# Kernel tuning notes

Hardware: AMD Instinct MI355X
Metric: run time of the kernel (lower is better)

## Reference

```python
import jax, jax.numpy as jnp
import numpy as np

N, IN_DIM, H1, NHEAD = 8192, 768, 128, 2
H1T = NHEAD * H1          # 256: each AttentionLayer output dim
H2, H3, OUT = 128, 128, 64
K = H1T + 1 - H2          # 129: conv kernel width
E_PAIRS = 100000
ALPHA = 0.2
NEG = -9e15


def _l2norm(x):
    # F.normalize(p=2, dim=1)
    return x / jnp.maximum(jnp.linalg.norm(x, axis=1, keepdims=True), 1e-12)


def _gat_block(h, adj_mask, a, act):
    # h: [N, D]; a: [2D, 1]; dense NxN GAT attention, masked softmax, aggregate
    D = h.shape[1]
    wh1 = h @ a[:D]            # [N,1]
    wh2 = h @ a[D:]            # [N,1]
    e = act(wh1 + wh2.T)       # [N,N]
    att = jnp.where(adj_mask, e, NEG)
    att = jax.nn.softmax(att, axis=1)   # dropout omitted (eval/deterministic)
    return att @ h             # [N,D]


def _attention_layer(x, adj_mask, W, a, b):
    h = x @ W                  # [N, H1T]
    hp = _gat_block(h, adj_mask, a, lambda z: jax.nn.leaky_relu(z, negative_slope=ALPHA))
    return _l2norm(jax.nn.elu(hp)) + b


def setup_inputs() -> dict:
    key = jax.random.key(0)
    ks = jax.random.split(key, 16)
    g = 1.414

    def xavier(k, shape):
        fan_in, fan_out = shape[-2], shape[-1]
        bound = g * np.sqrt(6.0 / (fan_in + fan_out))
        return jax.random.uniform(k, shape, jnp.float32, -bound, bound)

    x = jax.random.normal(ks[0], (N, IN_DIM), jnp.float32)
    adj = jax.random.randint(ks[1], (N, N), 0, 2, jnp.int32)
    train_sample = jax.random.randint(ks[2], (E_PAIRS, 2), 0, N, jnp.int32)

    return {
        "x": x, "adj": adj, "train_sample": train_sample,
        # per-head GAT params (stacked over heads)
        "head_W": xavier(ks[3], (NHEAD, IN_DIM, H1T)),
        "head_a": xavier(ks[4], (NHEAD, 2 * H1T, 1)),
        "head_b": jnp.zeros((NHEAD, H1T), jnp.float32),
        # Conv attention layer
        "conv_w": jax.random.normal(ks[5], (1, 1, 1, K), jnp.float32) * (1.0 / np.sqrt(K)),
        "conv_cb": jnp.zeros((1,), jnp.float32),
        "conv_a": xavier(ks[6], (2 * H2, 1)),
        "conv_b": jnp.zeros((H2,), jnp.float32),
        # decoder MLPs (stored as [in, out])
        "tf_w1": xavier(ks[7], (H2, H3)), "tf_b1": jnp.zeros((H3,), jnp.float32),
        "tf_w2": xavier(ks[8], (H3, OUT)), "tf_b2": jnp.zeros((OUT,), jnp.float32),
        "tg_w1": xavier(ks[9], (H2, H3)), "tg_b1": jnp.zeros((H3,), jnp.float32),
        "tg_w2": xavier(ks[10], (H3, OUT)), "tg_b2": jnp.zeros((OUT,), jnp.float32),
    }


def reference(x, adj, train_sample, head_W, head_a, head_b,
              conv_w, conv_cb, conv_a, conv_b,
              tf_w1, tf_b1, tf_w2, tf_b2, tg_w1, tg_b1, tg_w2, tg_b2):
    adj_mask = adj > 0

    # Layer 1: mean over attention heads, then elu
    heads = jax.vmap(_attention_layer, in_axes=(None, None, 0, 0, 0))(
        x, adj_mask, head_W, head_a, head_b)           # [NHEAD, N, H1T]
    z = jax.nn.elu(jnp.mean(heads, axis=0))            # [N, H1T]

    # Conv layer: 1x129 conv sliding over feature axis -> [N, H2]
    zi = z[None, None, :, :]                           # [1,1,N,H1T]
    hc = jax.lax.conv_general_dilated(
        zi, conv_w, window_strides=(1, 1), padding="VALID",
        dimension_numbers=("NCHW", "OIHW", "NCHW"))
    h = hc[0, 0] + conv_cb[0]                          # [N, H2]

    hp = _gat_block(h, adj_mask, conv_a, jax.nn.elu)
    embed = _l2norm(jax.nn.elu(hp)) + conv_b           # [N, H2]

    # decoders (dropout p=0.01 omitted for deterministic reference)
    tf = jax.nn.elu(jax.nn.elu(embed @ tf_w1 + tf_b1) @ tf_w2 + tf_b2)
    tg = jax.nn.elu(jax.nn.elu(embed @ tg_w1 + tg_b1) @ tg_w2 + tg_b2)

    pred = jnp.sum(tf[train_sample[:, 0]] * tg[train_sample[:, 1]], axis=1, keepdims=True)
    return pred
```

## Files before the change

kernel.cpp:

```cpp
#include <hip/hip_runtime.h>


typedef _Float16 f16;
typedef _Float16 f16x8 __attribute__((ext_vector_type(8)));
typedef float f32x4 __attribute__((ext_vector_type(4)));

#define DEV __device__ __forceinline__
#define L2E 1.4426950408889634f
#define NN 8192
#define IND 768
#define D1 256
#define DT 512
#define D2 128
#define KC 129
#define EPAIRS 100000

#if __has_builtin(__builtin_amdgcn_exp2f)
#define EXP2(x) __builtin_amdgcn_exp2f(x)
#else
#define EXP2(x) exp2f(x)
#endif

DEV float eluf(float x){ return x > 0.f ? x : EXP2(x*L2E) - 1.f; }

__global__ __launch_bounds__(256) void k_pack(const int4* __restrict__ adj4, unsigned* __restrict__ maskw){
  int idx = blockIdx.x*256 + threadIdx.x;
  int4 v = adj4[idx];
  unsigned n = (unsigned)(v.x > 0) | ((unsigned)(v.y > 0) << 1)
             | ((unsigned)(v.z > 0) << 2) | ((unsigned)(v.w > 0) << 3);
  n |= __shfl_xor(n, 1) << 4;
  n |= __shfl_xor(n, 2) << 8;
  n |= __shfl_xor(n, 4) << 16;
  if ((threadIdx.x & 7) == 0) maskw[idx >> 3] = n;
}

__global__ __launch_bounds__(256) void k_cast_x(const float* __restrict__ x, f16* __restrict__ x16){
  int i = (blockIdx.x*256 + threadIdx.x)*4;
  float4 v = *(const float4*)(x + i);
  union { f16 h[4]; uint2 u; } p;
  p.h[0]=(f16)v.x; p.h[1]=(f16)v.y; p.h[2]=(f16)v.z; p.h[3]=(f16)v.w;
  *(uint2*)(x16 + i) = p.u;
}

__global__ __launch_bounds__(256) void k_wt(const float* __restrict__ W, f16* __restrict__ Wt){
  int np = blockIdx.x; int h = np >> 8, d = np & 255;
  for (int k = threadIdx.x; k < IND; k += 256)
    Wt[(size_t)np*IND + k] = (f16)W[((size_t)h*IND + k)*D1 + d];
}

__global__ __launch_bounds__(256) void k_gemm_h(
    const f16* __restrict__ x16, const f16* __restrict__ Wt,
    const float* __restrict__ head_a,
    f16* __restrict__ hT, float* __restrict__ wh1, float* __restrict__ wh2){
  __shared__ f16 As[64*72];
  __shared__ f16 Bs[128*72];
  int m0 = blockIdx.x*64, n0 = blockIdx.y*128;
  int t = threadIdx.x, lane = t & 63, w = t >> 6;
  int wi = w >> 1, wd = w & 1;
  int rm = lane & 15, qm = (lane >> 4)*8;
  f32x4 acc[2][4] = {};
  for (int k0 = 0; k0 < IND; k0 += 64){
#pragma unroll
    for (int p = 0; p < 2; p++){
      int idx = p*256 + t, r = idx >> 3, cc = (idx & 7)*8;
      *(uint4*)&As[r*72 + cc] = *(const uint4*)&x16[(size_t)(m0 + r)*IND + k0 + cc];
    }
#pragma unroll
    for (int p = 0; p < 4; p++){
      int idx = p*256 + t, r = idx >> 3, cc = (idx & 7)*8;
      *(uint4*)&Bs[r*72 + cc] = *(const uint4*)&Wt[(size_t)(n0 + r)*IND + k0 + cc];
    }
    __syncthreads();
#pragma unroll
    for (int ks = 0; ks < 2; ks++){
      f16x8 a0 = *(const f16x8*)&As[(wi*32 + rm)*72 + ks*32 + qm];
      f16x8 a1 = *(const f16x8*)&As[(wi*32 + 16 + rm)*72 + ks*32 + qm];
#pragma unroll
      for (int fn = 0; fn < 4; fn++){
        f16x8 b = *(const f16x8*)&Bs[(wd*64 + fn*16 + rm)*72 + ks*32 + qm];
        acc[0][fn] = __builtin_amdgcn_mfma_f32_16x16x32_f16(a0, b, acc[0][fn], 0, 0, 0);
        acc[1][fn] = __builtin_amdgcn_mfma_f32_16x16x32_f16(a1, b, acc[1][fn], 0, 0, 0);
      }
    }
    __syncthreads();
  }
  int quad = lane >> 4, cl = lane & 15;
  int head = n0 >> 8;
  float a1v[4], a2v[4];
#pragma unroll
  for (int fn = 0; fn < 4; fn++){
    int d = (n0 & 255) + wd*64 + fn*16 + cl;
    a1v[fn] = head_a[head*DT + d];
    a2v[fn] = head_a[head*DT + D1 + d];
  }
  float p1[2][4], p2[2][4];
#pragma unroll
  for (int fi = 0; fi < 2; fi++){
#pragma unroll
    for (int fn = 0; fn < 4; fn++){
      int npg = n0 + wd*64 + fn*16 + cl;
      int mg = m0 + wi*32 + fi*16 + quad*4;
      union { f16 h[4]; uint2 u; } pk;
#pragma unroll
      for (int reg = 0; reg < 4; reg++) pk.h[reg] = (f16)acc[fi][fn][reg];
      *(uint2*)&hT[(size_t)npg*NN + mg] = pk.u;
    }
#pragma unroll
    for (int reg = 0; reg < 4; reg++){
      float s1 = 0.f, s2 = 0.f;
#pragma unroll
      for (int fn = 0; fn < 4; fn++){ s1 += acc[fi][fn][reg]*a1v[fn]; s2 += acc[fi][fn][reg]*a2v[fn]; }
      p1[fi][reg] = s1; p2[fi][reg] = s2;
    }
  }
#pragma unroll
  for (int o = 1; o < 16; o <<= 1){
#pragma unroll
    for (int fi = 0; fi < 2; fi++)
#pragma unroll
      for (int reg = 0; reg < 4; reg++){
        p1[fi][reg] += __shfl_xor(p1[fi][reg], o);
        p2[fi][reg] += __shfl_xor(p2[fi][reg], o);
      }
  }
  if (cl == 0){
#pragma unroll
    for (int fi = 0; fi < 2; fi++)
#pragma unroll
      for (int reg = 0; reg < 4; reg++){
        int mg = m0 + wi*32 + fi*16 + quad*4 + reg;
        atomicAdd(&wh1[head*NN + mg], p1[fi][reg]);
        atomicAdd(&wh2[head*NN + mg], p2[fi][reg]);
      }
  }
}

__global__ __launch_bounds__(256) void k_gmax(const float* __restrict__ wh2, unsigned* __restrict__ gmax){
  int h = blockIdx.y;
  int i = blockIdx.x*256 + threadIdx.x;
  float v = wh2[h*NN + i];
#pragma unroll
  for (int o = 32; o > 0; o >>= 1) v = fmaxf(v, __shfl_xor(v, o));
  if ((threadIdx.x & 63) == 0){
    unsigned b = __float_as_uint(v);
    unsigned enc = (b & 0x80000000u) ? ~b : (b | 0x80000000u);
    atomicMax(gmax + h, enc);
  }
}

__global__ __launch_bounds__(256) void k_colterms(const float* __restrict__ wh2,
                                                  float* __restrict__ c1, float* __restrict__ c2){
  int i = blockIdx.x*256 + threadIdx.x;
  float v = wh2[i]*L2E;
  c1[i] = v; c2[i] = 0.2f*v;
}

__global__ __launch_bounds__(256) void k_agg_head(
    const f16* __restrict__ hT, const unsigned* __restrict__ maskw,
    const float* __restrict__ wh1, const float* __restrict__ c1,
    const float* __restrict__ c2, const unsigned* __restrict__ gmaxp,
    float* __restrict__ num, float* __restrict__ den){
  __shared__ f16 Hs[256*72];
  __shared__ f16 Ws[64*72];
  __shared__ float rowa[64], rowb[64];
  int head = blockIdx.z;
  int i0 = blockIdx.x*64;
  int jbase = blockIdx.y*4096;
  const f16* hTh = hT + (size_t)head*D1*NN;
  int t = threadIdx.x, lane = t & 63, w = t >> 6;
  int rm = lane & 15, qm = (lane >> 4)*8;
  if (t < 64){
    unsigned e = gmaxp[head];
    float gmax = __uint_as_float((e & 0x80000000u) ? (e ^ 0x80000000u) : ~e);
    float u = wh1[head*NN + i0 + t];
    float sm = u + gmax;
    float M = (sm > 0.f ? sm : 0.2f*sm)*L2E;
    rowa[t] = u*L2E - M;
    rowb[t] = 0.2f*u*L2E - M;
  }
  __syncthreads();
  int si = t >> 2, sjq = (t & 3)*16;
  float ra = rowa[si], rb = rowb[si];
  const float* c1h = c1 + head*NN;
  const float* c2h = c2 + head*NN;
  const unsigned* mrowp = maskw + (size_t)(i0 + si)*(NN/32);
  float rden = 0.f;
  f32x4 acc[4][4] = {};
  for (int j0 = 0; j0 < 4096; j0 += 64){
    int jg = jbase + j0;
#pragma unroll
    for (int p = 0; p < 8; p++){
      int idx = p*256 + t, dr = idx >> 3, cc = (idx & 7)*8;
      *(uint4*)&Hs[dr*72 + cc] = *(const uint4*)&hTh[(size_t)dr*NN + jg + cc];
    }
    unsigned mb = mrowp[(jg + sjq) >> 5] >> (sjq & 31);
    float ca[16], cb[16];
#pragma unroll
    for (int k = 0; k < 4; k++){
      float4 va = *(const float4*)&c1h[jg + sjq + 4*k];
      float4 vb = *(const float4*)&c2h[jg + sjq + 4*k];
      ca[4*k]=va.x; ca[4*k+1]=va.y; ca[4*k+2]=va.z; ca[4*k+3]=va.w;
      cb[4*k]=vb.x; cb[4*k+1]=vb.y; cb[4*k+2]=vb.z; cb[4*k+3]=vb.w;
    }
    f16x8 wlo, whi;
    float dsum = 0.f;
#pragma unroll
    for (int q = 0; q < 16; q++){
      float s1 = ra + ca[q], s2 = rb + cb[q];
      float wv = EXP2(fmaxf(s1, s2));
      wv = ((mb >> q) & 1u) ? wv : 0.f;
      dsum += wv;
      if (q < 8) wlo[q] = (f16)wv; else whi[q - 8] = (f16)wv;
    }
    *(f16x8*)&Ws[si*72 + sjq]     = wlo;
    *(f16x8*)&Ws[si*72 + sjq + 8] = whi;
    dsum += __shfl_xor(dsum, 1);
    dsum += __shfl_xor(dsum, 2);
    rden += dsum;
    __syncthreads();
#pragma unroll
    for (int ks = 0; ks < 2; ks++){
      f16x8 a[4], b[4];
#pragma unroll
      for (int mi = 0; mi < 4; mi++) a[mi] = *(const f16x8*)&Ws[(mi*16 + rm)*72 + ks*32 + qm];
#pragma unroll
      for (int fn = 0; fn < 4; fn++) b[fn] = *(const f16x8*)&Hs[(w*64 + fn*16 + rm)*72 + ks*32 + qm];
#pragma unroll
      for (int mi = 0; mi < 4; mi++)
#pragma unroll
        for (int fn = 0; fn < 4; fn++)
          acc[mi][fn] = __builtin_amdgcn_mfma_f32_16x16x32_f16(a[mi], b[fn], acc[mi][fn], 0, 0, 0);
    }
    __syncthreads();
  }
  if ((t & 3) == 0) atomicAdd(&den[head*NN + i0 + si], rden);
  int quad = lane >> 4, cl = lane & 15;
#pragma unroll
  for (int mi = 0; mi < 4; mi++)
#pragma unroll
    for (int fn = 0; fn < 4; fn++){
      int rr = i0 + mi*16 + quad*4;
      int dc = w*64 + fn*16 + cl;
#pragma unroll
      for (int reg = 0; reg < 4; reg++)
        atomicAdd(&num[((size_t)head*NN + rr + reg)*D1 + dc], acc[mi][fn][reg]);
    }
}

__global__ __launch_bounds__(256) void k_merge_conv(
    const float* __restrict__ num, const float* __restrict__ den,
    const float* __restrict__ head_b, const float* __restrict__ conv_w,
    const float* __restrict__ conv_cb, const float* __restrict__ conv_a,
    f16* __restrict__ gT, float* __restrict__ wc1L, float* __restrict__ wc2L){
  __shared__ float zrow[2][256];
  __shared__ float cw[KC];
  __shared__ float ca[256];
  __shared__ float red[2][2];
  __shared__ float red2[2][2][2];
  int t = threadIdx.x, g = t >> 7, c = t & 127;
  int r = blockIdx.x*2 + g;
  if (t < KC) cw[t] = conv_w[t];
  ca[t] = conv_a[t];
  float zv0 = 0.f, zv1 = 0.f;
#pragma unroll
  for (int h = 0; h < 2; h++){
    const float* nr = num + ((size_t)h*NN + r)*D1;
    float inv = 1.f / den[h*NN + r];
    float e0 = eluf(nr[c]*inv);
    float e1 = eluf(nr[c + 128]*inv);
    float ss = e0*e0 + e1*e1;
#pragma unroll
    for (int o = 32; o > 0; o >>= 1) ss += __shfl_xor(ss, o);
    if ((t & 63) == 0) red[g][(t >> 6) & 1] = ss;
    __syncthreads();
    float invn = 1.f / fmaxf(sqrtf(red[g][0] + red[g][1]), 1e-12f);
    zv0 += e0*invn + head_b[h*D1 + c];
    zv1 += e1*invn + head_b[h*D1 + 128 + c];
    __syncthreads();
  }
  zrow[g][c]       = eluf(0.5f*zv0);
  zrow[g][c + 128] = eluf(0.5f*zv1);
  __syncthreads();
  float s = conv_cb[0];
  for (int k = 0; k < KC; k++) s += zrow[g][c + k]*cw[k];
  gT[(size_t)c*NN + r] = (f16)s;
  float p1 = s*ca[c], p2 = s*ca[128 + c];
#pragma unroll
  for (int o = 32; o > 0; o >>= 1){ p1 += __shfl_xor(p1, o); p2 += __shfl_xor(p2, o); }
  if ((t & 63) == 0){ red2[g][(t >> 6) & 1][0] = p1; red2[g][(t >> 6) & 1][1] = p2; }
  __syncthreads();
  if ((t & 127) == 0){
    wc1L[r] = (red2[g][0][0] + red2[g][1][0])*L2E;
    wc2L[r] = (red2[g][0][1] + red2[g][1][1])*L2E;
  }
}

__global__ __launch_bounds__(256) void k_agg_conv(
    const f16* __restrict__ gT, const unsigned* __restrict__ maskw,
    const float* __restrict__ wc1L, const float* __restrict__ wc2L,
    float* __restrict__ num, float* __restrict__ den){
  __shared__ f16 Hs[128*72];
  __shared__ f16 Ws[64*72];
  __shared__ float rowc[64];
  int i0 = blockIdx.x*64;
  int jbase = blockIdx.y*1024;
  int t = threadIdx.x, lane = t & 63, w = t >> 6;
  int rm = lane & 15, qm = (lane >> 4)*8;
  if (t < 64) rowc[t] = wc1L[i0 + t];
  __syncthreads();
  int si = t >> 2, sjq = (t & 3)*16;
  float ra = rowc[si];
  const unsigned* mrowp = maskw + (size_t)(i0 + si)*(NN/32);
  float rden = 0.f;
  f32x4 acc[4][2] = {};
  for (int j0 = 0; j0 < 1024; j0 += 64){
    int jg = jbase + j0;
#pragma unroll
    for (int p = 0; p < 4; p++){
      int idx = p*256 + t, dr = idx >> 3, cc = (idx & 7)*8;
      *(uint4*)&Hs[dr*72 + cc] = *(const uint4*)&gT[(size_t)dr*NN + jg + cc];
    }
    unsigned mb = mrowp[(jg + sjq) >> 5] >> (sjq & 31);
    float ca[16];
#pragma unroll
    for (int k = 0; k < 4; k++){
      float4 va = *(const float4*)&wc2L[jg + sjq + 4*k];
      ca[4*k]=va.x; ca[4*k+1]=va.y; ca[4*k+2]=va.z; ca[4*k+3]=va.w;
    }
    f16x8 wlo, whi;
    float dsum = 0.f;
#pragma unroll
    for (int q = 0; q < 16; q++){
      float sL = ra + ca[q];
      float t2 = EXP2(sL);
      float wv = sL > 0.f ? t2 : EXP2((t2 - 1.f)*L2E);
      wv = ((mb >> q) & 1u) ? wv : 0.f;
      dsum += wv;
      if (q < 8) wlo[q] = (f16)wv; else whi[q - 8] = (f16)wv;
    }
    *(f16x8*)&Ws[si*72 + sjq]     = wlo;
    *(f16x8*)&Ws[si*72 + sjq + 8] = whi;
    dsum += __shfl_xor(dsum, 1);
    dsum += __shfl_xor(dsum, 2);
    rden += dsum;
    __syncthreads();
#pragma unroll
    for (int ks = 0; ks < 2; ks++){
      f16x8 a[4], b[2];
#pragma unroll
      for (int mi = 0; mi < 4; mi++) a[mi] = *(const f16x8*)&Ws[(mi*16 + rm)*72 + ks*32 + qm];
#pragma unroll
      for (int fn = 0; fn < 2; fn++) b[fn] = *(const f16x8*)&Hs[(w*32 + fn*16 + rm)*72 + ks*32 + qm];
#pragma unroll
      for (int mi = 0; mi < 4; mi++)
#pragma unroll
        for (int fn = 0; fn < 2; fn++)
          acc[mi][fn] = __builtin_amdgcn_mfma_f32_16x16x32_f16(a[mi], b[fn], acc[mi][fn], 0, 0, 0);
    }
    __syncthreads();
  }
  if ((t & 3) == 0) atomicAdd(&den[i0 + si], rden);
  int quad = lane >> 4, cl = lane & 15;
#pragma unroll
  for (int mi = 0; mi < 4; mi++)
#pragma unroll
    for (int fn = 0; fn < 2; fn++){
      int rr = i0 + mi*16 + quad*4;
      int dc = w*32 + fn*16 + cl;
#pragma unroll
      for (int reg = 0; reg < 4; reg++)
        atomicAdd(&num[(size_t)(rr + reg)*D2 + dc], acc[mi][fn][reg]);
    }
}

__global__ __launch_bounds__(256) void k_embed(
    const float* __restrict__ numc, const float* __restrict__ denc,
    const float* __restrict__ conv_b, float* __restrict__ embed){
  __shared__ float red[2][2];
  int t = threadIdx.x, g = t >> 7, c = t & 127;
  int r = blockIdx.x*2 + g;
  float e = eluf(numc[(size_t)r*D2 + c] / denc[r]);
  float ss = e*e;
#pragma unroll
  for (int o = 32; o > 0; o >>= 1) ss += __shfl_xor(ss, o);
  if ((t & 63) == 0) red[g][(t >> 6) & 1] = ss;
  __syncthreads();
  float invn = 1.f / fmaxf(sqrtf(red[g][0] + red[g][1]), 1e-12f);
  embed[(size_t)r*D2 + c] = e*invn + conv_b[c];
}

__global__ __launch_bounds__(256) void k_mlp(
    const float* __restrict__ embed,
    const float* __restrict__ fw1, const float* __restrict__ fb1,
    const float* __restrict__ fw2, const float* __restrict__ fb2,
    const float* __restrict__ gw1, const float* __restrict__ gb1,
    const float* __restrict__ gw2, const float* __restrict__ gb2,
    float* __restrict__ tf, float* __restrict__ tg){
  const float* w1 = blockIdx.y ? gw1 : fw1;
  const float* b1 = blockIdx.y ? gb1 : fb1;
  const float* w2 = blockIdx.y ? gw2 : fw2;
  const float* b2 = blockIdx.y ? gb2 : fb2;
  float* out = blockIdx.y ? tg : tf;
  int t = threadIdx.x;
  int c = t & 127, kh = t >> 7;
  int o = t & 63, kh2 = t >> 6;
  float rw1[64];
#pragma unroll
  for (int i = 0; i < 64; i++) rw1[i] = w1[(kh*64 + i)*128 + c];
  float rw2[32];
#pragma unroll
  for (int i = 0; i < 32; i++) rw2[i] = w2[(kh2*32 + i)*64 + o];
  float bb1 = b1[c], bb2 = b2[o];
  __shared__ float erow[4][128];
  __shared__ float hidp[2][4][128];
  __shared__ float hid[4][128];
  __shared__ float outp[4][4][64];
  int r0 = blockIdx.x*32;
  for (int it = 0; it < 8; it++){
    int rbase = r0 + it*4;
    ((float2*)erow)[t] = ((const float2*)(embed + (size_t)rbase*128))[t];
    __syncthreads();
#pragma unroll
    for (int g = 0; g < 4; g++){
      float s = 0.f;
#pragma unroll
      for (int i = 0; i < 64; i++) s += erow[g][kh*64 + i]*rw1[i];
      hidp[kh][g][c] = s;
    }
    __syncthreads();
#pragma unroll
    for (int gg = 0; gg < 2; gg++){
      int g = kh + 2*gg;
      hid[g][c] = eluf(bb1 + hidp[0][g][c] + hidp[1][g][c]);
    }
    __syncthreads();
#pragma unroll
    for (int g = 0; g < 4; g++){
      float s = 0.f;
#pragma unroll
      for (int i = 0; i < 32; i++) s += hid[g][kh2*32 + i]*rw2[i];
      outp[kh2][g][o] = s;
    }
    __syncthreads();
    { int g = t >> 6;
      out[(size_t)(rbase + g)*64 + o] =
        eluf(bb2 + outp[0][g][o] + outp[1][g][o] + outp[2][g][o] + outp[3][g][o]); }
    __syncthreads();
  }
}

__global__ __launch_bounds__(256) void k_pred(
    const int* __restrict__ ts, const float4* __restrict__ tf4,
    const float4* __restrict__ tg4, float* __restrict__ out){
  int p = blockIdx.x*16 + (threadIdx.x >> 4);
  int l = threadIdx.x & 15;
  int i = ts[2*p], j = ts[2*p + 1];
  float4 a = tf4[(size_t)i*16 + l], b = tg4[(size_t)j*16 + l];
  float v = a.x*b.x + a.y*b.y + a.z*b.z + a.w*b.w;
  v += __shfl_xor(v, 1); v += __shfl_xor(v, 2);
  v += __shfl_xor(v, 4); v += __shfl_xor(v, 8);
  if (l == 0) out[p] = v;
}

#define OFF_MASK  ((size_t)0)
#define OFF_X16   ((size_t)8388608)
#define OFF_WT16  ((size_t)20971520)
#define OFF_HT16  ((size_t)21757952)
#define OFF_WH1   ((size_t)30146560)
#define OFF_WH2   ((size_t)30212096)
#define OFF_C1    ((size_t)30277632)
#define OFF_C2    ((size_t)30343168)
#define OFF_GMAX  ((size_t)30408704)
#define OFF_NUM1  ((size_t)30408960)
#define OFF_DEN1  ((size_t)47186176)
#define OFF_GT16  ((size_t)47251712)
#define OFF_WC1L  ((size_t)49348864)
#define OFF_WC2L  ((size_t)49381632)
#define OFF_NUMC  ((size_t)49414400)
#define OFF_DENC  ((size_t)53608704)
#define OFF_EMB   ((size_t)53641472)
#define OFF_TF    ((size_t)57835776)
#define OFF_TG    ((size_t)59932928)

extern "C" void kernel_launch(void* const* d_in, const int* in_sizes, int n_in,
                              void* d_out, int out_size, void* d_ws, size_t ws_size,
                              hipStream_t stream){
  const float* x      = (const float*)d_in[0];
  const int*   adj    = (const int*)d_in[1];
  const int*   ts     = (const int*)d_in[2];
  const float* head_W = (const float*)d_in[3];
  const float* head_a = (const float*)d_in[4];
  const float* head_b = (const float*)d_in[5];
  const float* conv_w = (const float*)d_in[6];
  const float* conv_cb= (const float*)d_in[7];
  const float* conv_a = (const float*)d_in[8];
  const float* conv_b = (const float*)d_in[9];
  const float* tf_w1  = (const float*)d_in[10];
  const float* tf_b1  = (const float*)d_in[11];
  const float* tf_w2  = (const float*)d_in[12];
  const float* tf_b2  = (const float*)d_in[13];
  const float* tg_w1  = (const float*)d_in[14];
  const float* tg_b1  = (const float*)d_in[15];
  const float* tg_w2  = (const float*)d_in[16];
  const float* tg_b2  = (const float*)d_in[17];
  float* outp = (float*)d_out;
  char* ws = (char*)d_ws;

  unsigned* maskw = (unsigned*)(ws + OFF_MASK);
  f16*   x16   = (f16*)(ws + OFF_X16);
  f16*   Wt16  = (f16*)(ws + OFF_WT16);
  f16*   hT16  = (f16*)(ws + OFF_HT16);
  float* wh1   = (float*)(ws + OFF_WH1);
  float* wh2   = (float*)(ws + OFF_WH2);
  float* c1    = (float*)(ws + OFF_C1);
  float* c2    = (float*)(ws + OFF_C2);
  unsigned* gmax = (unsigned*)(ws + OFF_GMAX);
  float* num1  = (float*)(ws + OFF_NUM1);
  float* den1  = (float*)(ws + OFF_DEN1);
  f16*   gT16  = (f16*)(ws + OFF_GT16);
  float* wc1L  = (float*)(ws + OFF_WC1L);
  float* wc2L  = (float*)(ws + OFF_WC2L);
  float* numc  = (float*)(ws + OFF_NUMC);
  float* denc  = (float*)(ws + OFF_DENC);
  float* emb   = (float*)(ws + OFF_EMB);
  float* tf    = (float*)(ws + OFF_TF);
  float* tg    = (float*)(ws + OFF_TG);

  hipMemsetAsync(wh1, 0, 2*2*NN*sizeof(float), stream);
  hipMemsetAsync(gmax, 0, 2*sizeof(unsigned), stream);
  hipMemsetAsync(num1, 0, (size_t)2*NN*D1*sizeof(float) + 2*NN*sizeof(float), stream);
  hipMemsetAsync(numc, 0, (size_t)NN*D2*sizeof(float) + NN*sizeof(float), stream);

  k_pack   <<<NN*NN/1024, 256, 0, stream>>>((const int4*)adj, maskw);
  k_cast_x <<<(NN*IND)/(256*4), 256, 0, stream>>>(x, x16);
  k_wt     <<<DT, 256, 0, stream>>>(head_W, Wt16);
  k_gemm_h <<<dim3(NN/64, DT/128), 256, 0, stream>>>(x16, Wt16, head_a, hT16, wh1, wh2);
  k_gmax   <<<dim3(NN/256, 2), 256, 0, stream>>>(wh2, gmax);
  k_colterms<<<(2*NN)/256, 256, 0, stream>>>(wh2, c1, c2);
  k_agg_head<<<dim3(NN/64, 2, 2), 256, 0, stream>>>(hT16, maskw, wh1, c1, c2, gmax, num1, den1);
  k_merge_conv<<<NN/2, 256, 0, stream>>>(num1, den1, head_b, conv_w, conv_cb, conv_a, gT16, wc1L, wc2L);
  k_agg_conv<<<dim3(NN/64, 8), 256, 0, stream>>>(gT16, maskw, wc1L, wc2L, numc, denc);
  k_embed  <<<NN/2, 256, 0, stream>>>(numc, denc, conv_b, emb);
  k_mlp    <<<dim3(NN/32, 2), 256, 0, stream>>>(emb, tf_w1, tf_b1, tf_w2, tf_b2,
                                                tg_w1, tg_b1, tg_w2, tg_b2, tf, tg);
  k_pred   <<<EPAIRS/16, 256, 0, stream>>>(ts, (const float4*)tf, (const float4*)tg, outp);
}
```

Measured before the change: 713.0 us.

## Load MFMA B operands directly from global and double-buffer attention weights in LDS

Both aggregation kernels stop staging the feature matrix tile in shared memory. Each lane now loads its MFMA B fragments straight from global/L2, and the attention-weight tile is double-buffered so the trailing barrier can go. The head kernel also splits the column range four ways instead of two and adds an occupancy hint of 4 blocks per CU. This cuts LDS traffic and barriers and raises occupancy, at the cost of more uncoalesced global reads per lane and more atomic adds for the partial results.

After: 802.6 us. +12.6%, slower.

```diff
diff --git a/kernel.cpp b/kernel.cpp
--- a/kernel.cpp
+++ b/kernel.cpp
@@ -14,6 +14,7 @@
 #define D2 128
 #define KC 129
 #define EPAIRS 100000
+#define JS1 4
 
 #if __has_builtin(__builtin_amdgcn_exp2f)
 #define EXP2(x) __builtin_amdgcn_exp2f(x)
@@ -155,17 +156,16 @@
   c1[i] = v; c2[i] = 0.2f*v;
 }
 
-__global__ __launch_bounds__(256) void k_agg_head(
+__global__ __launch_bounds__(256, 4) void k_agg_head(
     const f16* __restrict__ hT, const unsigned* __restrict__ maskw,
     const float* __restrict__ wh1, const float* __restrict__ c1,
     const float* __restrict__ c2, const unsigned* __restrict__ gmaxp,
     float* __restrict__ num, float* __restrict__ den){
-  __shared__ f16 Hs[256*72];
-  __shared__ f16 Ws[64*72];
+  __shared__ f16 Ws[2][64*72];
   __shared__ float rowa[64], rowb[64];
   int head = blockIdx.z;
   int i0 = blockIdx.x*64;
-  int jbase = blockIdx.y*4096;
+  int jbase = blockIdx.y*(NN/JS1);
   const f16* hTh = hT + (size_t)head*D1*NN;
   int t = threadIdx.x, lane = t & 63, w = t >> 6;
   int rm = lane & 15, qm = (lane >> 4)*8;
@@ -184,54 +184,66 @@
   const float* c1h = c1 + head*NN;
   const float* c2h = c2 + head*NN;
   const unsigned* mrowp = maskw + (size_t)(i0 + si)*(NN/32);
+  const f16* bp0 = hTh + (size_t)(w*64 +  0 + rm)*NN + qm;
+  const f16* bp1 = hTh + (size_t)(w*64 + 16 + rm)*NN + qm;
+  const f16* bp2 = hTh + (size_t)(w*64 + 32 + rm)*NN + qm;
+  const f16* bp3 = hTh + (size_t)(w*64 + 48 + rm)*NN + qm;
   float rden = 0.f;
   f32x4 acc[4][4] = {};
-  for (int j0 = 0; j0 < 4096; j0 += 64){
-    int jg = jbase + j0;
-#pragma unroll
-    for (int p = 0; p < 8; p++){
-      int idx = p*256 + t, dr = idx >> 3, cc = (idx & 7)*8;
-      *(uint4*)&Hs[dr*72 + cc] = *(const uint4*)&hTh[(size_t)dr*NN + jg + cc];
-    }
+  const int woff = si*72 + sjq;
+  for (int jt = 0; jt < (NN/JS1)/64; jt++){
+    int jg = jbase + jt*64;
+    f16* wsb = &Ws[jt & 1][0];
+    f16x8 b00 = *(const f16x8*)(bp0 + jg);
+    f16x8 b01 = *(const f16x8*)(bp1 + jg);
+    f16x8 b02 = *(const f16x8*)(bp2 + jg);
+    f16x8 b03 = *(const f16x8*)(bp3 + jg);
     unsigned mb = mrowp[(jg + sjq) >> 5] >> (sjq & 31);
-    float ca[16], cb[16];
+    f16x8 wlo, whi;
+    float dsum = 0.f;
 #pragma unroll
     for (int k = 0; k < 4; k++){
       float4 va = *(const float4*)&c1h[jg + sjq + 4*k];
       float4 vb = *(const float4*)&c2h[jg + sjq + 4*k];
-      ca[4*k]=va.x; ca[4*k+1]=va.y; ca[4*k+2]=va.z; ca[4*k+3]=va.w;
-      cb[4*k]=vb.x; cb[4*k+1]=vb.y; cb[4*k+2]=vb.z; cb[4*k+3]=vb.w;
-    }
-    f16x8 wlo, whi;
-    float dsum = 0.f;
-#pragma unroll
-    for (int q = 0; q < 16; q++){
-      float s1 = ra + ca[q], s2 = rb + cb[q];
-      float wv = EXP2(fmaxf(s1, s2));
-      wv = ((mb >> q) & 1u) ? wv : 0.f;
-      dsum += wv;
-      if (q < 8) wlo[q] = (f16)wv; else whi[q - 8] = (f16)wv;
-    }
-    *(f16x8*)&Ws[si*72 + sjq]     = wlo;
-    *(f16x8*)&Ws[si*72 + sjq + 8] = whi;
+      float w0 = EXP2(fmaxf(ra + va.x, rb + vb.x));
+      float w1 = EXP2(fmaxf(ra + va.y, rb + vb.y));
+      float w2 = EXP2(fmaxf(ra + va.z, rb + vb.z));
+      float w3 = EXP2(fmaxf(ra + va.w, rb + vb.w));
+      w0 = ((mb >> (4*k + 0)) & 1u) ? w0 : 0.f;
+      w1 = ((mb >> (4*k + 1)) & 1u) ? w1 : 0.f;
+      w2 = ((mb >> (4*k + 2)) & 1u) ? w2 : 0.f;
+      w3 = ((mb >> (4*k + 3)) & 1u) ? w3 : 0.f;
+      dsum += (w0 + w1) + (w2 + w3);
+      if (k < 2){
+        wlo[4*k]=(f16)w0; wlo[4*k+1]=(f16)w1; wlo[4*k+2]=(f16)w2; wlo[4*k+3]=(f16)w3;
+      } else {
+        whi[4*k-8]=(f16)w0; whi[4*k-7]=(f16)w1; whi[4*k-6]=(f16)w2; whi[4*k-5]=(f16)w3;
+      }
+    }
+    *(f16x8*)&wsb[woff]     = wlo;
+    *(f16x8*)&wsb[woff + 8] = whi;
     dsum += __shfl_xor(dsum, 1);
     dsum += __shfl_xor(dsum, 2);
     rden += dsum;
     __syncthreads();
+    f16x8 b10 = *(const f16x8*)(bp0 + jg + 32);
+    f16x8 b11 = *(const f16x8*)(bp1 + jg + 32);
+    f16x8 b12 = *(const f16x8*)(bp2 + jg + 32);
+    f16x8 b13 = *(const f16x8*)(bp3 + jg + 32);
 #pragma unroll
     for (int ks = 0; ks < 2; ks++){
-      f16x8 a[4], b[4];
-#pragma unroll
-      for (int mi = 0; mi < 4; mi++) a[mi] = *(const f16x8*)&Ws[(mi*16 + rm)*72 + ks*32 + qm];
-#pragma unroll
-      for (int fn = 0; fn < 4; fn++) b[fn] = *(const f16x8*)&Hs[(w*64 + fn*16 + rm)*72 + ks*32 + qm];
+      f16x8 a[4];
+#pragma unroll
+      for (int mi = 0; mi < 4; mi++) a[mi] = *(const f16x8*)&wsb[(mi*16 + rm)*72 + ks*32 + qm];
+      f16x8 b[4];
+      b[0] = ks ? b10 : b00; b[1] = ks ? b11 : b01;
+      b[2] = ks ? b12 : b02; b[3] = ks ? b13 : b03;
 #pragma unroll
       for (int mi = 0; mi < 4; mi++)
 #pragma unroll
         for (int fn = 0; fn < 4; fn++)
           acc[mi][fn] = __builtin_amdgcn_mfma_f32_16x16x32_f16(a[mi], b[fn], acc[mi][fn], 0, 0, 0);
     }
-    __syncthreads();
   }
   if ((t & 3) == 0) atomicAdd(&den[head*NN + i0 + si], rden);
   int quad = lane >> 4, cl = lane & 15;
@@ -295,12 +307,11 @@
   }
 }
 
-__global__ __launch_bounds__(256) void k_agg_conv(
+__global__ __launch_bounds__(256, 4) void k_agg_conv(
     const f16* __restrict__ gT, const unsigned* __restrict__ maskw,
     const float* __restrict__ wc1L, const float* __restrict__ wc2L,
     float* __restrict__ num, float* __restrict__ den){
-  __shared__ f16 Hs[128*72];
-  __shared__ f16 Ws[64*72];
+  __shared__ f16 Ws[2][64*72];
   __shared__ float rowc[64];
   int i0 = blockIdx.x*64;
   int jbase = blockIdx.y*1024;
@@ -311,53 +322,60 @@
   int si = t >> 2, sjq = (t & 3)*16;
   float ra = rowc[si];
   const unsigned* mrowp = maskw + (size_t)(i0 + si)*(NN/32);
+  const f16* bp0 = gT + (size_t)(w*32 +  0 + rm)*NN + qm;
+  const f16* bp1 = gT + (size_t)(w*32 + 16 + rm)*NN + qm;
   float rden = 0.f;
   f32x4 acc[4][2] = {};
-  for (int j0 = 0; j0 < 1024; j0 += 64){
-    int jg = jbase + j0;
-#pragma unroll
-    for (int p = 0; p < 4; p++){
-      int idx = p*256 + t, dr = idx >> 3, cc = (idx & 7)*8;
-      *(uint4*)&Hs[dr*72 + cc] = *(const uint4*)&gT[(size_t)dr*NN + jg + cc];
-    }
+  const int woff = si*72 + sjq;
+  for (int jt = 0; jt < 16; jt++){
+    int jg = jbase + jt*64;
+    f16* wsb = &Ws[jt & 1][0];
+    f16x8 b00 = *(const f16x8*)(bp0 + jg);
+    f16x8 b01 = *(const f16x8*)(bp1 + jg);
     unsigned mb = mrowp[(jg + sjq) >> 5] >> (sjq & 31);
-    float ca[16];
+    f16x8 wlo, whi;
+    float dsum = 0.f;
 #pragma unroll
     for (int k = 0; k < 4; k++){
       float4 va = *(const float4*)&wc2L[jg + sjq + 4*k];
-      ca[4*k]=va.x; ca[4*k+1]=va.y; ca[4*k+2]=va.z; ca[4*k+3]=va.w;
-    }
-    f16x8 wlo, whi;
-    float dsum = 0.f;
-#pragma unroll
-    for (int q = 0; q < 16; q++){
-      float sL = ra + ca[q];
-      float t2 = EXP2(sL);
-      float wv = sL > 0.f ? t2 : EXP2((t2 - 1.f)*L2E);
-      wv = ((mb >> q) & 1u) ? wv : 0.f;
-      dsum += wv;
-      if (q < 8) wlo[q] = (f16)wv; else whi[q - 8] = (f16)wv;
-    }
-    *(f16x8*)&Ws[si*72 + sjq]     = wlo;
-    *(f16x8*)&Ws[si*72 + sjq + 8] = whi;
+      float sL0 = ra + va.x, sL1 = ra + va.y, sL2 = ra + va.z, sL3 = ra + va.w;
+      float t20 = EXP2(sL0), t21 = EXP2(sL1), t22 = EXP2(sL2), t23 = EXP2(sL3);
+      float w0 = sL0 > 0.f ? t20 : EXP2((t20 - 1.f)*L2E);
+      float w1 = sL1 > 0.f ? t21 : EXP2((t21 - 1.f)*L2E);
+      float w2 = sL2 > 0.f ? t22 : EXP2((t22 - 1.f)*L2E);
+      float w3 = sL3 > 0.f ? t23 : EXP2((t23 - 1.f)*L2E);
+      w0 = ((mb >> (4*k + 0)) & 1u) ? w0 : 0.f;
+      w1 = ((mb >> (4*k + 1)) & 1u) ? w1 : 0.f;
+      w2 = ((mb >> (4*k + 2)) & 1u) ? w2 : 0.f;
+      w3 = ((mb >> (4*k + 3)) & 1u) ? w3 : 0.f;
+      dsum += (w0 + w1) + (w2 + w3);
+      if (k < 2){
+        wlo[4*k]=(f16)w0; wlo[4*k+1]=(f16)w1; wlo[4*k+2]=(f16)w2; wlo[4*k+3]=(f16)w3;
+      } else {
+        whi[4*k-8]=(f16)w0; whi[4*k-7]=(f16)w1; whi[4*k-6]=(f16)w2; whi[4*k-5]=(f16)w3;
+      }
+    }
+    *(f16x8*)&wsb[woff]     = wlo;
+    *(f16x8*)&wsb[woff + 8] = whi;
     dsum += __shfl_xor(dsum, 1);
     dsum += __shfl_xor(dsum, 2);
     rden += dsum;
     __syncthreads();
+    f16x8 b10 = *(const f16x8*)(bp0 + jg + 32);
+    f16x8 b11 = *(const f16x8*)(bp1 + jg + 32);
 #pragma unroll
     for (int ks = 0; ks < 2; ks++){
-      f16x8 a[4], b[2];
-#pragma unroll
-      for (int mi = 0; mi < 4; mi++) a[mi] = *(const f16x8*)&Ws[(mi*16 + rm)*72 + ks*32 + qm];
-#pragma unroll
-      for (int fn = 0; fn < 2; fn++) b[fn] = *(const f16x8*)&Hs[(w*32 + fn*16 + rm)*72 + ks*32 + qm];
+      f16x8 a[4];
+#pragma unroll
+      for (int mi = 0; mi < 4; mi++) a[mi] = *(const f16x8*)&wsb[(mi*16 + rm)*72 + ks*32 + qm];
+      f16x8 b[2];
+      b[0] = ks ? b10 : b00; b[1] = ks ? b11 : b01;
 #pragma unroll
       for (int mi = 0; mi < 4; mi++)
 #pragma unroll
         for (int fn = 0; fn < 2; fn++)
           acc[mi][fn] = __builtin_amdgcn_mfma_f32_16x16x32_f16(a[mi], b[fn], acc[mi][fn], 0, 0, 0);
     }
-    __syncthreads();
   }
   if ((t & 3) == 0) atomicAdd(&den[i0 + si], rden);
   int quad = lane >> 4, cl = lane & 15;
@@ -537,7 +555,7 @@
   k_gemm_h <<<dim3(NN/64, DT/128), 256, 0, stream>>>(x16, Wt16, head_a, hT16, wh1, wh2);
   k_gmax   <<<dim3(NN/256, 2), 256, 0, stream>>>(wh2, gmax);
   k_colterms<<<(2*NN)/256, 256, 0, stream>>>(wh2, c1, c2);
-  k_agg_head<<<dim3(NN/64, 2, 2), 256, 0, stream>>>(hT16, maskw, wh1, c1, c2, gmax, num1, den1);
+  k_agg_head<<<dim3(NN/64, JS1, 2), 256, 0, stream>>>(hT16, maskw, wh1, c1, c2, gmax, num1, den1);
   k_merge_conv<<<NN/2, 256, 0, stream>>>(num1, den1, head_b, conv_w, conv_cb, conv_a, gT16, wc1L, wc2L);
   k_agg_conv<<<dim3(NN/64, 8), 256, 0, stream>>>(gT16, maskw, wc1L, wc2L, numc, denc);
   k_embed  <<<NN/2, 256, 0, stream>>>(numc, denc, conv_b, emb);
```
